# Kernel optimization log

Measured on AMD Instinct MI355X. Metric: run time of the kernel, lower is better.

Reference implementation:

```python
import jax, jax.numpy as jnp
import numpy as np

B0 = 2048
B1 = 2048


def _param(k, shape, fan_in):
    return jax.random.normal(k, shape, dtype=jnp.float32) / np.float32(np.sqrt(fan_in))


def setup_inputs() -> dict:
    key = jax.random.key(0)
    ks = jax.random.split(key, 32)
    inp = {
        'zw_0': jax.random.normal(ks[0], (B0, 128), dtype=jnp.float32),
        'zw_1': jax.random.normal(ks[1], (B1, 128), dtype=jnp.float32),
        'c': jax.random.normal(ks[2], (B0 + B1, 64), dtype=jnp.float32),
        # Wk: Linear(64 -> 128)
        'Wk_w': _param(ks[3], (128, 64), 64), 'Wk_b': jnp.zeros((128,), jnp.float32),
        # Ww[0], Ww[1]: Linear(64 -> 128)
        'Ww0_w': _param(ks[4], (128, 64), 64), 'Ww0_b': jnp.zeros((128,), jnp.float32),
        'Ww1_w': _param(ks[5], (128, 64), 64), 'Ww1_b': jnp.zeros((128,), jnp.float32),
        # linear_0/1: Linear(128 -> 64) + ReLU
        'lin0_w': _param(ks[6], (64, 128), 128), 'lin0_b': jnp.zeros((64,), jnp.float32),
        'lin1_w': _param(ks[7], (64, 128), 128), 'lin1_b': jnp.zeros((64,), jnp.float32),
        # attention_0/1: Linear(64->32), Tanh, Linear(32->1)
        'a0_1w': _param(ks[8], (32, 64), 64), 'a0_1b': jnp.zeros((32,), jnp.float32),
        'a0_2w': _param(ks[9], (1, 32), 32), 'a0_2b': jnp.zeros((1,), jnp.float32),
        'a1_1w': _param(ks[10], (32, 64), 64), 'a1_1b': jnp.zeros((32,), jnp.float32),
        'a1_2w': _param(ks[11], (1, 32), 32), 'a1_2b': jnp.zeros((1,), jnp.float32),
    }
    return inp


def _loo_pool(zw, lw, lb, a1w, a1b, a2w, a2b):
    # zt = ReLU(Linear(128->64))  [B, 64]
    zt = jax.nn.relu(zw @ lw.T + lb)
    # attention score per row  [B]
    s = (jnp.tanh(zt @ a1w.T + a1b) @ a2w.T + a2b)[:, 0]
    B = zt.shape[0]
    # leave-one-out softmax: row i attends over all j != i (diag masked to -inf)
    logits = jnp.where(jnp.eye(B, dtype=bool), -jnp.inf, jnp.broadcast_to(s[None, :], (B, B)))
    w = jax.nn.softmax(logits, axis=1)  # [B, B]
    return w @ zt  # [B, 64]


def reference(zw_0, zw_1, c,
              Wk_w, Wk_b, Ww0_w, Ww0_b, Ww1_w, Ww1_b,
              lin0_w, lin0_b, lin1_w, lin1_b,
              a0_1w, a0_1b, a0_2w, a0_2b,
              a1_1w, a1_1b, a1_2w, a1_2b):
    b0 = zw_0.shape[0]
    pooled0 = _loo_pool(zw_0, lin0_w, lin0_b, a0_1w, a0_1b, a0_2w, a0_2b)
    pooled1 = _loo_pool(zw_1, lin1_w, lin1_b, a1_1w, a1_1b, a1_2w, a1_2b)
    ck = c @ Wk_w.T + Wk_b  # [B, 128]
    pred0 = pooled0 @ Ww0_w.T + Ww0_b + ck[:b0]
    pred1 = pooled1 @ Ww1_w.T + Ww1_b + ck[b0:]
    pred = jnp.concatenate([pred0, pred1], axis=0)  # [B, 128]
    zw = jnp.concatenate([zw_0, zw_1], axis=0)      # [B, 128]
    total = zw @ pred.T                              # [B, B]
    batch = total.shape[0]
    nce_w = -jnp.sum(jnp.diagonal(jax.nn.log_softmax(total, axis=1))) / batch
    return nce_w
```

## Files before the change

kernel.cpp:

```cpp
#include <hip/hip_runtime.h>
#include <math.h>

#define B_TOT 4096
#define B_HALF 2048

#define ZT_OFF     0
#define S_OFF      262144
#define STATS_OFF  266240
#define ZWB_OFF    524288
#define PREDB_OFF  786432
#define ROWVAL_OFF 1048576

typedef __bf16 bf16x8 __attribute__((ext_vector_type(8)));
typedef float  f32x4  __attribute__((ext_vector_type(4)));

__device__ __forceinline__ unsigned short f2bf(float f) {
    unsigned u = __float_as_uint(f);
    u = u + 0x7fffu + ((u >> 16) & 1u);
    return (unsigned short)(u >> 16);
}
__device__ __forceinline__ float bf2f(unsigned short h) {
    return __uint_as_float(((unsigned)h) << 16);
}

__global__ __launch_bounds__(256)
void k_zt_s(const float* __restrict__ zw0, const float* __restrict__ zw1,
            const float* __restrict__ lin0_w, const float* __restrict__ lin0_b,
            const float* __restrict__ lin1_w, const float* __restrict__ lin1_b,
            const float* __restrict__ a0_1w, const float* __restrict__ a0_1b,
            const float* __restrict__ a0_2w, const float* __restrict__ a0_2b,
            const float* __restrict__ a1_1w, const float* __restrict__ a1_1b,
            const float* __restrict__ a1_2w, const float* __restrict__ a1_2b,
            float* __restrict__ ws) {
    __shared__ float lws[64 * 132];
    __shared__ float zws[16 * 132];
    __shared__ float ztl[16 * 68];
    __shared__ float a1s[32 * 68];
    int tid = threadIdx.x;
    int base = blockIdx.x * 16;
    int g = (base >= B_HALF);
    const float* lw = g ? lin1_w : lin0_w;
    const float* lb = g ? lin1_b : lin0_b;
    const float* w1 = g ? a1_1w : a0_1w;
    const float* b1 = g ? a1_1b : a0_1b;
    const float* w2 = g ? a1_2w : a0_2w;
    const float* b2 = g ? a1_2b : a0_2b;
    unsigned short* zwb = (unsigned short*)(ws + ZWB_OFF);

    const float4* lw4 = (const float4*)lw;
    for (int i = tid; i < 2048; i += 256) {
        int o = i >> 5, k4 = i & 31;
        ((float4*)(lws + o * 132))[k4] = lw4[i];
    }
    for (int i = tid; i < 512; i += 256) {
        int r = i >> 5, k4 = i & 31;
        int gi = base + r;
        const float* zr = (gi < B_HALF) ? (zw0 + (size_t)gi * 128)
                                        : (zw1 + (size_t)(gi - B_HALF) * 128);
        float4 v = ((const float4*)zr)[k4];
        ((float4*)(zws + r * 132))[k4] = v;
        uint2 p;
        p.x = (unsigned)f2bf(v.x) | ((unsigned)f2bf(v.y) << 16);
        p.y = (unsigned)f2bf(v.z) | ((unsigned)f2bf(v.w) << 16);
        ((uint2*)(zwb + (size_t)gi * 128))[k4] = p;
    }
    const float4* w14 = (const float4*)w1;
    for (int i = tid; i < 512; i += 256) {
        int o = i >> 4, k4 = i & 15;
        ((float4*)(a1s + o * 68))[k4] = w14[i];
    }
    __syncthreads();

    int o = tid & 63, rgrp = tid >> 6;
    {
        float bias = lb[o];
        float acc[4] = {bias, bias, bias, bias};
        const float4* wrow = (const float4*)(lws + o * 132);
        const float4* zr0 = (const float4*)(zws + (rgrp + 0) * 132);
        const float4* zr1 = (const float4*)(zws + (rgrp + 4) * 132);
        const float4* zr2 = (const float4*)(zws + (rgrp + 8) * 132);
        const float4* zr3 = (const float4*)(zws + (rgrp + 12) * 132);
#pragma unroll 4
        for (int k4 = 0; k4 < 32; ++k4) {
            float4 wv = wrow[k4];
            float4 z0 = zr0[k4], z1 = zr1[k4], z2 = zr2[k4], z3 = zr3[k4];
            acc[0] = fmaf(wv.x, z0.x, fmaf(wv.y, z0.y, fmaf(wv.z, z0.z, fmaf(wv.w, z0.w, acc[0]))));
            acc[1] = fmaf(wv.x, z1.x, fmaf(wv.y, z1.y, fmaf(wv.z, z1.z, fmaf(wv.w, z1.w, acc[1]))));
            acc[2] = fmaf(wv.x, z2.x, fmaf(wv.y, z2.y, fmaf(wv.z, z2.z, fmaf(wv.w, z2.w, acc[2]))));
            acc[3] = fmaf(wv.x, z3.x, fmaf(wv.y, z3.y, fmaf(wv.z, z3.z, fmaf(wv.w, z3.w, acc[3]))));
        }
#pragma unroll
        for (int rr = 0; rr < 4; ++rr) {
            int row = rgrp + rr * 4;
            float zt = fmaxf(acc[rr], 0.f);
            ztl[row * 68 + o] = zt;
            ws[ZT_OFF + (size_t)(base + row) * 64 + o] = zt;
        }
    }
    __syncthreads();

    int o2 = tid & 31, r2 = tid >> 5;
    const float4* arow = (const float4*)(a1s + o2 * 68);
#pragma unroll
    for (int rpass = 0; rpass < 2; ++rpass) {
        int row = r2 + rpass * 8;
        float a = b1[o2];
        const float4* zt4 = (const float4*)(ztl + row * 68);
#pragma unroll 4
        for (int k4 = 0; k4 < 16; ++k4) {
            float4 wv = arow[k4];
            float4 zv = zt4[k4];
            a = fmaf(wv.x, zv.x, fmaf(wv.y, zv.y, fmaf(wv.z, zv.z, fmaf(wv.w, zv.w, a))));
        }
        float h = tanhf(a) * w2[o2];
#pragma unroll
        for (int mask = 16; mask > 0; mask >>= 1) h += __shfl_xor(h, mask);
        if (o2 == 0) ws[S_OFF + base + row] = h + b2[0];
    }
}

__global__ __launch_bounds__(1024)
void k_stats(float* __restrict__ ws) {
    __shared__ float red[1024];
    __shared__ float el[B_HALF];
    __shared__ float tl[16 * 64];
    int gg = blockIdx.x, tid = threadIdx.x;
    const float* sg = ws + S_OFF + gg * B_HALF;

    float m = -INFINITY;
    for (int r = tid; r < B_HALF; r += 1024) m = fmaxf(m, sg[r]);
    red[tid] = m;
    __syncthreads();
    for (int o = 512; o > 0; o >>= 1) {
        if (tid < o) red[tid] = fmaxf(red[tid], red[tid + o]);
        __syncthreads();
    }
    m = red[0];
    __syncthreads();

    float Eloc = 0.f;
    for (int r = tid; r < B_HALF; r += 1024) {
        float ev = __expf(sg[r] - m);
        el[r] = ev;
        Eloc += ev;
    }
    red[tid] = Eloc;
    __syncthreads();
    for (int o = 512; o > 0; o >>= 1) {
        if (tid < o) red[tid] += red[tid + o];
        __syncthreads();
    }
    float E = red[0];

    int sub = tid >> 6, d = tid & 63;
    const float* ztg = ws + ZT_OFF + (size_t)gg * B_HALF * 64;
    float t = 0.f;
    for (int r = sub; r < B_HALF; r += 16) t = fmaf(el[r], ztg[(size_t)r * 64 + d], t);
    tl[sub * 64 + d] = t;
    __syncthreads();
    if (tid < 64) {
        float tt = 0.f;
#pragma unroll
        for (int q = 0; q < 16; ++q) tt += tl[q * 64 + tid];
        ws[STATS_OFF + gg * 66 + 2 + tid] = tt;
    }
    if (tid == 0) {
        ws[STATS_OFF + gg * 66]     = m;
        ws[STATS_OFF + gg * 66 + 1] = E;
    }
}

__global__ __launch_bounds__(256)
void k_pred(const float* __restrict__ c,
            const float* __restrict__ Wk_w, const float* __restrict__ Wk_b,
            const float* __restrict__ Ww0_w, const float* __restrict__ Ww0_b,
            const float* __restrict__ Ww1_w, const float* __restrict__ Ww1_b,
            float* __restrict__ ws) {
    __shared__ float Wws[128 * 68];
    __shared__ float Wks[128 * 68];
    __shared__ float pl[16 * 68];
    __shared__ float cl[16 * 68];
    __shared__ float er_l[16], inv_l[16];
    int tid = threadIdx.x;
    int base = blockIdx.x * 16;
    int g = (base >= B_HALF);
    const float* Ww  = g ? Ww1_w : Ww0_w;
    const float* Wwb = g ? Ww1_b : Ww0_b;
    unsigned short* predb = (unsigned short*)(ws + PREDB_OFF);

    const float4* Ww4 = (const float4*)Ww;
    const float4* Wk4 = (const float4*)Wk_w;
    for (int i = tid; i < 2048; i += 256) {
        int o = i >> 4, k4 = i & 15;
        ((float4*)(Wws + o * 68))[k4] = Ww4[i];
        ((float4*)(Wks + o * 68))[k4] = Wk4[i];
    }
    for (int i = tid; i < 256; i += 256) {
        int r = i >> 4, k4 = i & 15;
        ((float4*)(cl + r * 68))[k4] = ((const float4*)(c + (size_t)(base + r) * 64))[k4];
    }
    if (tid < 16) {
        float m = ws[STATS_OFF + g * 66];
        float E = ws[STATS_OFF + g * 66 + 1];
        float er = __expf(ws[S_OFF + base + tid] - m);
        er_l[tid] = er;
        inv_l[tid] = 1.f / (E - er);
    }
    __syncthreads();
    for (int i = tid; i < 1024; i += 256) {
        int r = i >> 6, k = i & 63;
        float T = ws[STATS_OFF + g * 66 + 2 + k];
        float zt = ws[ZT_OFF + (size_t)(base + r) * 64 + k];
        pl[r * 68 + k] = (T - er_l[r] * zt) * inv_l[r];
    }
    __syncthreads();

    int o = tid & 127, rsel = tid >> 7;
    float bias = Wwb[o] + Wk_b[o];
    float acc[8] = {bias, bias, bias, bias, bias, bias, bias, bias};
    const float4* wrow = (const float4*)(Wws + o * 68);
    const float4* krow = (const float4*)(Wks + o * 68);
#pragma unroll 4
    for (int k4 = 0; k4 < 16; ++k4) {
        float4 wv = wrow[k4];
#pragma unroll
        for (int j = 0; j < 8; ++j) {
            float4 pv = ((const float4*)(pl + (rsel + j * 2) * 68))[k4];
            acc[j] = fmaf(wv.x, pv.x, fmaf(wv.y, pv.y, fmaf(wv.z, pv.z, fmaf(wv.w, pv.w, acc[j]))));
        }
    }
#pragma unroll 4
    for (int k4 = 0; k4 < 16; ++k4) {
        float4 kv = krow[k4];
#pragma unroll
        for (int j = 0; j < 8; ++j) {
            float4 cv = ((const float4*)(cl + (rsel + j * 2) * 68))[k4];
            acc[j] = fmaf(kv.x, cv.x, fmaf(kv.y, cv.y, fmaf(kv.z, cv.z, fmaf(kv.w, cv.w, acc[j]))));
        }
    }
#pragma unroll
    for (int j = 0; j < 8; ++j) {
        int gi = base + rsel + j * 2;
        predb[(size_t)gi * 128 + o] = f2bf(acc[j]);
    }
}

__global__ __launch_bounds__(256)
void k_main(float* __restrict__ ws) {
    __shared__ unsigned short zs[64 * 136];
    __shared__ unsigned short ps[64 * 136];
    int tid = threadIdx.x;
    int jx = blockIdx.x;
    int i0 = blockIdx.y * 64, j0 = jx * 64;
    const unsigned short* zwb   = (const unsigned short*)(ws + ZWB_OFF);
    const unsigned short* predb = (const unsigned short*)(ws + PREDB_OFF);

    for (int i = tid; i < 1024; i += 256) {
        int r = i >> 4, gq = i & 15;
        ((float4*)(zs + r * 136))[gq] = ((const float4*)(zwb + (size_t)(i0 + r) * 128))[gq];
        ((float4*)(ps + r * 136))[gq] = ((const float4*)(predb + (size_t)(j0 + r) * 128))[gq];
    }
    __syncthreads();

    int lane = tid & 63, w = tid >> 6;
    int m16 = lane & 15, quad = lane >> 4;

    bf16x8 af[4];
#pragma unroll
    for (int kk = 0; kk < 4; ++kk)
        af[kk] = *((const bf16x8*)(zs + (w * 16 + m16) * 136 + kk * 32 + quad * 8));

    f32x4 acc[4];
#pragma unroll
    for (int b = 0; b < 4; ++b) acc[b] = (f32x4){0.f, 0.f, 0.f, 0.f};

#pragma unroll
    for (int b = 0; b < 4; ++b) {
#pragma unroll
        for (int kk = 0; kk < 4; ++kk) {
            bf16x8 bf = *((const bf16x8*)(ps + (b * 16 + m16) * 136 + kk * 32 + quad * 8));
            acc[b] = __builtin_amdgcn_mfma_f32_16x16x32_bf16(af[kk], bf, acc[b], 0, 0, 0);
        }
    }

    float2* part = (float2*)ws;
#pragma unroll
    for (int r = 0; r < 4; ++r) {
        float vm = fmaxf(fmaxf(acc[0][r], acc[1][r]), fmaxf(acc[2][r], acc[3][r]));
#pragma unroll
        for (int mask = 8; mask > 0; mask >>= 1) vm = fmaxf(vm, __shfl_xor(vm, mask));
        float se = __expf(acc[0][r] - vm) + __expf(acc[1][r] - vm) +
                   __expf(acc[2][r] - vm) + __expf(acc[3][r] - vm);
#pragma unroll
        for (int mask = 8; mask > 0; mask >>= 1) se += __shfl_xor(se, mask);
        if (m16 == 0) {
            int gi = i0 + w * 16 + quad * 4 + r;
            part[(size_t)gi * 64 + jx] = make_float2(vm, se);
        }
    }
}

__global__ __launch_bounds__(256)
void k_row(const float* __restrict__ zw0, const float* __restrict__ zw1,
           float* __restrict__ ws) {
    int tid = threadIdx.x;
    int sub = tid >> 6, lane = tid & 63;
    int r = blockIdx.x * 4 + sub;
    const float2* part = (const float2*)ws;
    const unsigned short* predb = (const unsigned short*)(ws + PREDB_OFF);

    float2 p2 = part[(size_t)r * 64 + lane];
    float M = p2.x, S = p2.y;
#pragma unroll
    for (int mask = 32; mask > 0; mask >>= 1) M = fmaxf(M, __shfl_xor(M, mask));
    S = S * __expf(p2.x - M);
#pragma unroll
    for (int mask = 32; mask > 0; mask >>= 1) S += __shfl_xor(S, mask);

    const float* zr = (r < B_HALF) ? (zw0 + (size_t)r * 128)
                                   : (zw1 + (size_t)(r - B_HALF) * 128);
    const unsigned short* pr = predb + (size_t)r * 128;
    float d = zr[lane] * bf2f(pr[lane]) + zr[lane + 64] * bf2f(pr[lane + 64]);
#pragma unroll
    for (int mask = 32; mask > 0; mask >>= 1) d += __shfl_xor(d, mask);

    if (lane == 0) ws[ROWVAL_OFF + r] = d - (M + logf(S));
}

__global__ __launch_bounds__(1024)
void k_final(const float* __restrict__ ws, float* __restrict__ out) {
    __shared__ float red[1024];
    int tid = threadIdx.x;
    float a = 0.f;
    for (int r = tid; r < B_TOT; r += 1024) a += ws[ROWVAL_OFF + r];
    red[tid] = a;
    __syncthreads();
    for (int o = 512; o > 0; o >>= 1) {
        if (tid < o) red[tid] += red[tid + o];
        __syncthreads();
    }
    if (tid == 0) out[0] = -red[0] / (float)B_TOT;
}

extern "C" void kernel_launch(void* const* d_in, const int* in_sizes, int n_in,
                              void* d_out, int out_size, void* d_ws, size_t ws_size,
                              hipStream_t stream) {
    const float* zw_0   = (const float*)d_in[0];
    const float* zw_1   = (const float*)d_in[1];
    const float* c      = (const float*)d_in[2];
    const float* Wk_w   = (const float*)d_in[3];
    const float* Wk_b   = (const float*)d_in[4];
    const float* Ww0_w  = (const float*)d_in[5];
    const float* Ww0_b  = (const float*)d_in[6];
    const float* Ww1_w  = (const float*)d_in[7];
    const float* Ww1_b  = (const float*)d_in[8];
    const float* lin0_w = (const float*)d_in[9];
    const float* lin0_b = (const float*)d_in[10];
    const float* lin1_w = (const float*)d_in[11];
    const float* lin1_b = (const float*)d_in[12];
    const float* a0_1w  = (const float*)d_in[13];
    const float* a0_1b  = (const float*)d_in[14];
    const float* a0_2w  = (const float*)d_in[15];
    const float* a0_2b  = (const float*)d_in[16];
    const float* a1_1w  = (const float*)d_in[17];
    const float* a1_1b  = (const float*)d_in[18];
    const float* a1_2w  = (const float*)d_in[19];
    const float* a1_2b  = (const float*)d_in[20];
    float* ws  = (float*)d_ws;
    float* out = (float*)d_out;

    k_zt_s<<<256, 256, 0, stream>>>(zw_0, zw_1, lin0_w, lin0_b, lin1_w, lin1_b,
                                    a0_1w, a0_1b, a0_2w, a0_2b,
                                    a1_1w, a1_1b, a1_2w, a1_2b, ws);
    k_stats<<<2, 1024, 0, stream>>>(ws);
    k_pred<<<256, 256, 0, stream>>>(c, Wk_w, Wk_b, Ww0_w, Ww0_b, Ww1_w, Ww1_b, ws);
    k_main<<<dim3(64, 64), 256, 0, stream>>>(ws);
    k_row<<<1024, 256, 0, stream>>>(zw_0, zw_1, ws);
    k_final<<<1, 1024, 0, stream>>>(ws, out);
}
```

Before: 172.4 us.

## Fuse all stages into one cooperative persistent kernel with grid syncs

Replaces the six separate kernel launches with a single cooperative kernel of 256 blocks that separates its stages with grid.sync. The softmax statistics are now per-block partial sums of exp(s) taken without max subtraction, which removes the serial two-block stats kernel. The main logits GEMM has each block stream 1024 columns with double-buffered LDS tiles and an online max/sum, and the final reduction uses an atomicAdd. This cuts launch overhead and serial small kernels, but it needs cooperative launch, runs only 256 blocks for the GEMM, and risks overflow because the exponentials are no longer max-stabilised.

After: 273.2 us. 58.4% more time.

```diff
diff --git a/kernel.cpp b/kernel.cpp
--- a/kernel.cpp
+++ b/kernel.cpp
@@ -1,15 +1,20 @@
 #include <hip/hip_runtime.h>
+#include <hip/hip_cooperative_groups.h>
 #include <math.h>
+
+namespace cg = cooperative_groups;
 
 #define B_TOT 4096
 #define B_HALF 2048
+#define NBLK 256
 
 #define ZT_OFF     0
 #define S_OFF      262144
-#define STATS_OFF  266240
+#define PSTAT_OFF  266240
 #define ZWB_OFF    524288
 #define PREDB_OFF  786432
-#define ROWVAL_OFF 1048576
+#define PART_OFF   1048576
+#define ACC_OFF    1081344
 
 typedef __bf16 bf16x8 __attribute__((ext_vector_type(8)));
 typedef float  f32x4  __attribute__((ext_vector_type(4)));
@@ -23,323 +28,325 @@
     return __uint_as_float(((unsigned)h) << 16);
 }
 
-__global__ __launch_bounds__(256)
-void k_zt_s(const float* __restrict__ zw0, const float* __restrict__ zw1,
-            const float* __restrict__ lin0_w, const float* __restrict__ lin0_b,
-            const float* __restrict__ lin1_w, const float* __restrict__ lin1_b,
-            const float* __restrict__ a0_1w, const float* __restrict__ a0_1b,
-            const float* __restrict__ a0_2w, const float* __restrict__ a0_2b,
-            const float* __restrict__ a1_1w, const float* __restrict__ a1_1b,
-            const float* __restrict__ a1_2w, const float* __restrict__ a1_2b,
-            float* __restrict__ ws) {
-    __shared__ float lws[64 * 132];
-    __shared__ float zws[16 * 132];
-    __shared__ float ztl[16 * 68];
-    __shared__ float a1s[32 * 68];
+__global__ __launch_bounds__(256, 1)
+void k_fused(const float* __restrict__ zw0, const float* __restrict__ zw1,
+             const float* __restrict__ c,
+             const float* __restrict__ Wk_w, const float* __restrict__ Wk_b,
+             const float* __restrict__ Ww0_w, const float* __restrict__ Ww0_b,
+             const float* __restrict__ Ww1_w, const float* __restrict__ Ww1_b,
+             const float* __restrict__ lin0_w, const float* __restrict__ lin0_b,
+             const float* __restrict__ lin1_w, const float* __restrict__ lin1_b,
+             const float* __restrict__ a0_1w, const float* __restrict__ a0_1b,
+             const float* __restrict__ a0_2w, const float* __restrict__ a0_2b,
+             const float* __restrict__ a1_1w, const float* __restrict__ a1_1b,
+             const float* __restrict__ a1_2w, const float* __restrict__ a1_2b,
+             float* __restrict__ ws, float* __restrict__ out) {
+    __shared__ float smem[20480];
+    cg::grid_group grid = cg::this_grid();
     int tid = threadIdx.x;
-    int base = blockIdx.x * 16;
-    int g = (base >= B_HALF);
-    const float* lw = g ? lin1_w : lin0_w;
-    const float* lb = g ? lin1_b : lin0_b;
-    const float* w1 = g ? a1_1w : a0_1w;
-    const float* b1 = g ? a1_1b : a0_1b;
-    const float* w2 = g ? a1_2w : a0_2w;
-    const float* b2 = g ? a1_2b : a0_2b;
-    unsigned short* zwb = (unsigned short*)(ws + ZWB_OFF);
-
-    const float4* lw4 = (const float4*)lw;
-    for (int i = tid; i < 2048; i += 256) {
-        int o = i >> 5, k4 = i & 31;
-        ((float4*)(lws + o * 132))[k4] = lw4[i];
-    }
-    for (int i = tid; i < 512; i += 256) {
-        int r = i >> 5, k4 = i & 31;
-        int gi = base + r;
-        const float* zr = (gi < B_HALF) ? (zw0 + (size_t)gi * 128)
-                                        : (zw1 + (size_t)(gi - B_HALF) * 128);
-        float4 v = ((const float4*)zr)[k4];
-        ((float4*)(zws + r * 132))[k4] = v;
-        uint2 p;
-        p.x = (unsigned)f2bf(v.x) | ((unsigned)f2bf(v.y) << 16);
-        p.y = (unsigned)f2bf(v.z) | ((unsigned)f2bf(v.w) << 16);
-        ((uint2*)(zwb + (size_t)gi * 128))[k4] = p;
-    }
-    const float4* w14 = (const float4*)w1;
-    for (int i = tid; i < 512; i += 256) {
-        int o = i >> 4, k4 = i & 15;
-        ((float4*)(a1s + o * 68))[k4] = w14[i];
-    }
-    __syncthreads();
-
-    int o = tid & 63, rgrp = tid >> 6;
+    int b = blockIdx.x;
+    unsigned short* zwb   = (unsigned short*)(ws + ZWB_OFF);
+    unsigned short* predb = (unsigned short*)(ws + PREDB_OFF);
+
     {
-        float bias = lb[o];
-        float acc[4] = {bias, bias, bias, bias};
-        const float4* wrow = (const float4*)(lws + o * 132);
-        const float4* zr0 = (const float4*)(zws + (rgrp + 0) * 132);
-        const float4* zr1 = (const float4*)(zws + (rgrp + 4) * 132);
-        const float4* zr2 = (const float4*)(zws + (rgrp + 8) * 132);
-        const float4* zr3 = (const float4*)(zws + (rgrp + 12) * 132);
+        float* lws = smem;
+        float* zws = smem + 8448;
+        float* ztl = smem + 10560;
+        float* a1s = smem + 11648;
+        float* el  = smem + 13824;
+        int base = b * 16;
+        int g = (base >= B_HALF);
+        const float* lw = g ? lin1_w : lin0_w;
+        const float* lb = g ? lin1_b : lin0_b;
+        const float* w1 = g ? a1_1w : a0_1w;
+        const float* b1 = g ? a1_1b : a0_1b;
+        const float* w2 = g ? a1_2w : a0_2w;
+        const float* b2 = g ? a1_2b : a0_2b;
+
+        const float4* lw4 = (const float4*)lw;
+        for (int i = tid; i < 2048; i += 256) {
+            int o = i >> 5, k4 = i & 31;
+            ((float4*)(lws + o * 132))[k4] = lw4[i];
+        }
+        for (int i = tid; i < 512; i += 256) {
+            int r = i >> 5, k4 = i & 31;
+            int gi = base + r;
+            const float* zr = (gi < B_HALF) ? (zw0 + (size_t)gi * 128)
+                                            : (zw1 + (size_t)(gi - B_HALF) * 128);
+            float4 v = ((const float4*)zr)[k4];
+            ((float4*)(zws + r * 132))[k4] = v;
+            uint2 p;
+            p.x = (unsigned)f2bf(v.x) | ((unsigned)f2bf(v.y) << 16);
+            p.y = (unsigned)f2bf(v.z) | ((unsigned)f2bf(v.w) << 16);
+            ((uint2*)(zwb + (size_t)gi * 128))[k4] = p;
+        }
+        const float4* w14 = (const float4*)w1;
+        for (int i = tid; i < 512; i += 256) {
+            int o = i >> 4, k4 = i & 15;
+            ((float4*)(a1s + o * 68))[k4] = w14[i];
+        }
+        __syncthreads();
+
+        int o = tid & 63, rgrp = tid >> 6;
+        {
+            float bias = lb[o];
+            float acc[4] = {bias, bias, bias, bias};
+            const float4* wrow = (const float4*)(lws + o * 132);
+            const float4* zr0 = (const float4*)(zws + (rgrp + 0) * 132);
+            const float4* zr1 = (const float4*)(zws + (rgrp + 4) * 132);
+            const float4* zr2 = (const float4*)(zws + (rgrp + 8) * 132);
+            const float4* zr3 = (const float4*)(zws + (rgrp + 12) * 132);
 #pragma unroll 4
-        for (int k4 = 0; k4 < 32; ++k4) {
-            float4 wv = wrow[k4];
-            float4 z0 = zr0[k4], z1 = zr1[k4], z2 = zr2[k4], z3 = zr3[k4];
-            acc[0] = fmaf(wv.x, z0.x, fmaf(wv.y, z0.y, fmaf(wv.z, z0.z, fmaf(wv.w, z0.w, acc[0]))));
-            acc[1] = fmaf(wv.x, z1.x, fmaf(wv.y, z1.y, fmaf(wv.z, z1.z, fmaf(wv.w, z1.w, acc[1]))));
-            acc[2] = fmaf(wv.x, z2.x, fmaf(wv.y, z2.y, fmaf(wv.z, z2.z, fmaf(wv.w, z2.w, acc[2]))));
-            acc[3] = fmaf(wv.x, z3.x, fmaf(wv.y, z3.y, fmaf(wv.z, z3.z, fmaf(wv.w, z3.w, acc[3]))));
-        }
-#pragma unroll
-        for (int rr = 0; rr < 4; ++rr) {
-            int row = rgrp + rr * 4;
-            float zt = fmaxf(acc[rr], 0.f);
-            ztl[row * 68 + o] = zt;
-            ws[ZT_OFF + (size_t)(base + row) * 64 + o] = zt;
-        }
-    }
-    __syncthreads();
-
-    int o2 = tid & 31, r2 = tid >> 5;
-    const float4* arow = (const float4*)(a1s + o2 * 68);
-#pragma unroll
-    for (int rpass = 0; rpass < 2; ++rpass) {
-        int row = r2 + rpass * 8;
-        float a = b1[o2];
-        const float4* zt4 = (const float4*)(ztl + row * 68);
+            for (int k4 = 0; k4 < 32; ++k4) {
+                float4 wv = wrow[k4];
+                float4 z0 = zr0[k4], z1 = zr1[k4], z2 = zr2[k4], z3 = zr3[k4];
+                acc[0] = fmaf(wv.x, z0.x, fmaf(wv.y, z0.y, fmaf(wv.z, z0.z, fmaf(wv.w, z0.w, acc[0]))));
+                acc[1] = fmaf(wv.x, z1.x, fmaf(wv.y, z1.y, fmaf(wv.z, z1.z, fmaf(wv.w, z1.w, acc[1]))));
+                acc[2] = fmaf(wv.x, z2.x, fmaf(wv.y, z2.y, fmaf(wv.z, z2.z, fmaf(wv.w, z2.w, acc[2]))));
+                acc[3] = fmaf(wv.x, z3.x, fmaf(wv.y, z3.y, fmaf(wv.z, z3.z, fmaf(wv.w, z3.w, acc[3]))));
+            }
+#pragma unroll
+            for (int rr = 0; rr < 4; ++rr) {
+                int row = rgrp + rr * 4;
+                float zt = fmaxf(acc[rr], 0.f);
+                ztl[row * 68 + o] = zt;
+                ws[ZT_OFF + (size_t)(base + row) * 64 + o] = zt;
+            }
+        }
+        __syncthreads();
+
+        int o2 = tid & 31, r2 = tid >> 5;
+        const float4* arow = (const float4*)(a1s + o2 * 68);
+#pragma unroll
+        for (int rpass = 0; rpass < 2; ++rpass) {
+            int row = r2 + rpass * 8;
+            float a = b1[o2];
+            const float4* zt4 = (const float4*)(ztl + row * 68);
+#pragma unroll 4
+            for (int k4 = 0; k4 < 16; ++k4) {
+                float4 wv = arow[k4];
+                float4 zv = zt4[k4];
+                a = fmaf(wv.x, zv.x, fmaf(wv.y, zv.y, fmaf(wv.z, zv.z, fmaf(wv.w, zv.w, a))));
+            }
+            float h = tanhf(a) * w2[o2];
+#pragma unroll
+            for (int mask = 16; mask > 0; mask >>= 1) h += __shfl_xor(h, mask);
+            if (o2 == 0) {
+                float e = __expf(h + b2[0]);
+                el[row] = e;
+                ws[S_OFF + base + row] = e;
+            }
+        }
+        __syncthreads();
+
+        if (tid < 64) {
+            float t = 0.f;
+#pragma unroll
+            for (int r = 0; r < 16; ++r) t = fmaf(el[r], ztl[r * 68 + tid], t);
+            ws[PSTAT_OFF + b * 65 + 1 + tid] = t;
+        }
+        if (tid == 64) {
+            float E = 0.f;
+#pragma unroll
+            for (int r = 0; r < 16; ++r) E += el[r];
+            ws[PSTAT_OFF + b * 65] = E;
+        }
+        if (b == 0 && tid == 0) ws[ACC_OFF] = 0.f;
+    }
+    grid.sync();
+
+    {
+        float* Wws = smem;
+        float* Wks = smem + 8704;
+        float* pl  = smem + 17408;
+        float* cl  = smem + 18496;
+        float* Ts  = smem + 19584;
+        int base = b * 16;
+        int g = (b >= 128);
+        const float* Ww  = g ? Ww1_w : Ww0_w;
+        const float* Wwb = g ? Ww1_b : Ww0_b;
+
+        const float4* Ww4 = (const float4*)Ww;
+        const float4* Wk4 = (const float4*)Wk_w;
+        for (int i = tid; i < 2048; i += 256) {
+            int o = i >> 4, k4 = i & 15;
+            ((float4*)(Wws + o * 68))[k4] = Ww4[i];
+            ((float4*)(Wks + o * 68))[k4] = Wk4[i];
+        }
+        if (tid < 256) {
+            int r = tid >> 4, k4 = tid & 15;
+            ((float4*)(cl + r * 68))[k4] = ((const float4*)(c + (size_t)(base + r) * 64))[k4];
+        }
+        if (tid < 65) {
+            float t = 0.f;
+            const float* ps = ws + PSTAT_OFF + (size_t)g * 128 * 65 + tid;
+            for (int q = 0; q < 128; ++q) t += ps[(size_t)q * 65];
+            Ts[tid] = t;
+        }
+        __syncthreads();
+        for (int i = tid; i < 1024; i += 256) {
+            int r = i >> 6, k = i & 63;
+            float er = ws[S_OFF + base + r];
+            pl[r * 68 + k] = (Ts[1 + k] - er * ws[ZT_OFF + (size_t)(base + r) * 64 + k])
+                             / (Ts[0] - er);
+        }
+        __syncthreads();
+
+        int o = tid & 127, rsel = tid >> 7;
+        float bias = Wwb[o] + Wk_b[o];
+        float acc[8] = {bias, bias, bias, bias, bias, bias, bias, bias};
+        const float4* wrow = (const float4*)(Wws + o * 68);
+        const float4* krow = (const float4*)(Wks + o * 68);
 #pragma unroll 4
         for (int k4 = 0; k4 < 16; ++k4) {
-            float4 wv = arow[k4];
-            float4 zv = zt4[k4];
-            a = fmaf(wv.x, zv.x, fmaf(wv.y, zv.y, fmaf(wv.z, zv.z, fmaf(wv.w, zv.w, a))));
-        }
-        float h = tanhf(a) * w2[o2];
-#pragma unroll
-        for (int mask = 16; mask > 0; mask >>= 1) h += __shfl_xor(h, mask);
-        if (o2 == 0) ws[S_OFF + base + row] = h + b2[0];
-    }
-}
-
-__global__ __launch_bounds__(1024)
-void k_stats(float* __restrict__ ws) {
-    __shared__ float red[1024];
-    __shared__ float el[B_HALF];
-    __shared__ float tl[16 * 64];
-    int gg = blockIdx.x, tid = threadIdx.x;
-    const float* sg = ws + S_OFF + gg * B_HALF;
-
-    float m = -INFINITY;
-    for (int r = tid; r < B_HALF; r += 1024) m = fmaxf(m, sg[r]);
-    red[tid] = m;
-    __syncthreads();
-    for (int o = 512; o > 0; o >>= 1) {
-        if (tid < o) red[tid] = fmaxf(red[tid], red[tid + o]);
-        __syncthreads();
-    }
-    m = red[0];
-    __syncthreads();
-
-    float Eloc = 0.f;
-    for (int r = tid; r < B_HALF; r += 1024) {
-        float ev = __expf(sg[r] - m);
-        el[r] = ev;
-        Eloc += ev;
-    }
-    red[tid] = Eloc;
-    __syncthreads();
-    for (int o = 512; o > 0; o >>= 1) {
-        if (tid < o) red[tid] += red[tid + o];
-        __syncthreads();
-    }
-    float E = red[0];
-
-    int sub = tid >> 6, d = tid & 63;
-    const float* ztg = ws + ZT_OFF + (size_t)gg * B_HALF * 64;
-    float t = 0.f;
-    for (int r = sub; r < B_HALF; r += 16) t = fmaf(el[r], ztg[(size_t)r * 64 + d], t);
-    tl[sub * 64 + d] = t;
-    __syncthreads();
-    if (tid < 64) {
-        float tt = 0.f;
-#pragma unroll
-        for (int q = 0; q < 16; ++q) tt += tl[q * 64 + tid];
-        ws[STATS_OFF + gg * 66 + 2 + tid] = tt;
-    }
-    if (tid == 0) {
-        ws[STATS_OFF + gg * 66]     = m;
-        ws[STATS_OFF + gg * 66 + 1] = E;
-    }
-}
-
-__global__ __launch_bounds__(256)
-void k_pred(const float* __restrict__ c,
-            const float* __restrict__ Wk_w, const float* __restrict__ Wk_b,
-            const float* __restrict__ Ww0_w, const float* __restrict__ Ww0_b,
-            const float* __restrict__ Ww1_w, const float* __restrict__ Ww1_b,
-            float* __restrict__ ws) {
-    __shared__ float Wws[128 * 68];
-    __shared__ float Wks[128 * 68];
-    __shared__ float pl[16 * 68];
-    __shared__ float cl[16 * 68];
-    __shared__ float er_l[16], inv_l[16];
-    int tid = threadIdx.x;
-    int base = blockIdx.x * 16;
-    int g = (base >= B_HALF);
-    const float* Ww  = g ? Ww1_w : Ww0_w;
-    const float* Wwb = g ? Ww1_b : Ww0_b;
-    unsigned short* predb = (unsigned short*)(ws + PREDB_OFF);
-
-    const float4* Ww4 = (const float4*)Ww;
-    const float4* Wk4 = (const float4*)Wk_w;
-    for (int i = tid; i < 2048; i += 256) {
-        int o = i >> 4, k4 = i & 15;
-        ((float4*)(Wws + o * 68))[k4] = Ww4[i];
-        ((float4*)(Wks + o * 68))[k4] = Wk4[i];
-    }
-    for (int i = tid; i < 256; i += 256) {
-        int r = i >> 4, k4 = i & 15;
-        ((float4*)(cl + r * 68))[k4] = ((const float4*)(c + (size_t)(base + r) * 64))[k4];
-    }
-    if (tid < 16) {
-        float m = ws[STATS_OFF + g * 66];
-        float E = ws[STATS_OFF + g * 66 + 1];
-        float er = __expf(ws[S_OFF + base + tid] - m);
-        er_l[tid] = er;
-        inv_l[tid] = 1.f / (E - er);
-    }
-    __syncthreads();
-    for (int i = tid; i < 1024; i += 256) {
-        int r = i >> 6, k = i & 63;
-        float T = ws[STATS_OFF + g * 66 + 2 + k];
-        float zt = ws[ZT_OFF + (size_t)(base + r) * 64 + k];
-        pl[r * 68 + k] = (T - er_l[r] * zt) * inv_l[r];
-    }
-    __syncthreads();
-
-    int o = tid & 127, rsel = tid >> 7;
-    float bias = Wwb[o] + Wk_b[o];
-    float acc[8] = {bias, bias, bias, bias, bias, bias, bias, bias};
-    const float4* wrow = (const float4*)(Wws + o * 68);
-    const float4* krow = (const float4*)(Wks + o * 68);
+            float4 wv = wrow[k4];
+#pragma unroll
+            for (int j = 0; j < 8; ++j) {
+                float4 pv = ((const float4*)(pl + (rsel + j * 2) * 68))[k4];
+                acc[j] = fmaf(wv.x, pv.x, fmaf(wv.y, pv.y, fmaf(wv.z, pv.z, fmaf(wv.w, pv.w, acc[j]))));
+            }
+        }
 #pragma unroll 4
-    for (int k4 = 0; k4 < 16; ++k4) {
-        float4 wv = wrow[k4];
-#pragma unroll
-        for (int j = 0; j < 8; ++j) {
-            float4 pv = ((const float4*)(pl + (rsel + j * 2) * 68))[k4];
-            acc[j] = fmaf(wv.x, pv.x, fmaf(wv.y, pv.y, fmaf(wv.z, pv.z, fmaf(wv.w, pv.w, acc[j]))));
-        }
-    }
-#pragma unroll 4
-    for (int k4 = 0; k4 < 16; ++k4) {
-        float4 kv = krow[k4];
-#pragma unroll
-        for (int j = 0; j < 8; ++j) {
-            float4 cv = ((const float4*)(cl + (rsel + j * 2) * 68))[k4];
-            acc[j] = fmaf(kv.x, cv.x, fmaf(kv.y, cv.y, fmaf(kv.z, cv.z, fmaf(kv.w, cv.w, acc[j]))));
-        }
-    }
-#pragma unroll
-    for (int j = 0; j < 8; ++j) {
-        int gi = base + rsel + j * 2;
-        predb[(size_t)gi * 128 + o] = f2bf(acc[j]);
-    }
-}
-
-__global__ __launch_bounds__(256)
-void k_main(float* __restrict__ ws) {
-    __shared__ unsigned short zs[64 * 136];
-    __shared__ unsigned short ps[64 * 136];
-    int tid = threadIdx.x;
-    int jx = blockIdx.x;
-    int i0 = blockIdx.y * 64, j0 = jx * 64;
-    const unsigned short* zwb   = (const unsigned short*)(ws + ZWB_OFF);
-    const unsigned short* predb = (const unsigned short*)(ws + PREDB_OFF);
-
-    for (int i = tid; i < 1024; i += 256) {
-        int r = i >> 4, gq = i & 15;
-        ((float4*)(zs + r * 136))[gq] = ((const float4*)(zwb + (size_t)(i0 + r) * 128))[gq];
-        ((float4*)(ps + r * 136))[gq] = ((const float4*)(predb + (size_t)(j0 + r) * 128))[gq];
-    }
-    __syncthreads();
-
-    int lane = tid & 63, w = tid >> 6;
-    int m16 = lane & 15, quad = lane >> 4;
-
-    bf16x8 af[4];
-#pragma unroll
-    for (int kk = 0; kk < 4; ++kk)
-        af[kk] = *((const bf16x8*)(zs + (w * 16 + m16) * 136 + kk * 32 + quad * 8));
-
-    f32x4 acc[4];
-#pragma unroll
-    for (int b = 0; b < 4; ++b) acc[b] = (f32x4){0.f, 0.f, 0.f, 0.f};
-
-#pragma unroll
-    for (int b = 0; b < 4; ++b) {
-#pragma unroll
-        for (int kk = 0; kk < 4; ++kk) {
-            bf16x8 bf = *((const bf16x8*)(ps + (b * 16 + m16) * 136 + kk * 32 + quad * 8));
-            acc[b] = __builtin_amdgcn_mfma_f32_16x16x32_bf16(af[kk], bf, acc[b], 0, 0, 0);
-        }
-    }
-
-    float2* part = (float2*)ws;
-#pragma unroll
-    for (int r = 0; r < 4; ++r) {
-        float vm = fmaxf(fmaxf(acc[0][r], acc[1][r]), fmaxf(acc[2][r], acc[3][r]));
-#pragma unroll
-        for (int mask = 8; mask > 0; mask >>= 1) vm = fmaxf(vm, __shfl_xor(vm, mask));
-        float se = __expf(acc[0][r] - vm) + __expf(acc[1][r] - vm) +
-                   __expf(acc[2][r] - vm) + __expf(acc[3][r] - vm);
-#pragma unroll
-        for (int mask = 8; mask > 0; mask >>= 1) se += __shfl_xor(se, mask);
-        if (m16 == 0) {
-            int gi = i0 + w * 16 + quad * 4 + r;
-            part[(size_t)gi * 64 + jx] = make_float2(vm, se);
-        }
-    }
-}
-
-__global__ __launch_bounds__(256)
-void k_row(const float* __restrict__ zw0, const float* __restrict__ zw1,
-           float* __restrict__ ws) {
-    int tid = threadIdx.x;
-    int sub = tid >> 6, lane = tid & 63;
-    int r = blockIdx.x * 4 + sub;
-    const float2* part = (const float2*)ws;
-    const unsigned short* predb = (const unsigned short*)(ws + PREDB_OFF);
-
-    float2 p2 = part[(size_t)r * 64 + lane];
-    float M = p2.x, S = p2.y;
-#pragma unroll
-    for (int mask = 32; mask > 0; mask >>= 1) M = fmaxf(M, __shfl_xor(M, mask));
-    S = S * __expf(p2.x - M);
-#pragma unroll
-    for (int mask = 32; mask > 0; mask >>= 1) S += __shfl_xor(S, mask);
-
-    const float* zr = (r < B_HALF) ? (zw0 + (size_t)r * 128)
-                                   : (zw1 + (size_t)(r - B_HALF) * 128);
-    const unsigned short* pr = predb + (size_t)r * 128;
-    float d = zr[lane] * bf2f(pr[lane]) + zr[lane + 64] * bf2f(pr[lane + 64]);
-#pragma unroll
-    for (int mask = 32; mask > 0; mask >>= 1) d += __shfl_xor(d, mask);
-
-    if (lane == 0) ws[ROWVAL_OFF + r] = d - (M + logf(S));
-}
-
-__global__ __launch_bounds__(1024)
-void k_final(const float* __restrict__ ws, float* __restrict__ out) {
-    __shared__ float red[1024];
-    int tid = threadIdx.x;
-    float a = 0.f;
-    for (int r = tid; r < B_TOT; r += 1024) a += ws[ROWVAL_OFF + r];
-    red[tid] = a;
-    __syncthreads();
-    for (int o = 512; o > 0; o >>= 1) {
-        if (tid < o) red[tid] += red[tid + o];
-        __syncthreads();
-    }
-    if (tid == 0) out[0] = -red[0] / (float)B_TOT;
+        for (int k4 = 0; k4 < 16; ++k4) {
+            float4 kv = krow[k4];
+#pragma unroll
+            for (int j = 0; j < 8; ++j) {
+                float4 cv = ((const float4*)(cl + (rsel + j * 2) * 68))[k4];
+                acc[j] = fmaf(kv.x, cv.x, fmaf(kv.y, cv.y, fmaf(kv.z, cv.z, fmaf(kv.w, cv.w, acc[j]))));
+            }
+        }
+#pragma unroll
+        for (int j = 0; j < 8; ++j)
+            predb[(size_t)(base + rsel + j * 2) * 128 + o] = f2bf(acc[j]);
+    }
+    grid.sync();
+
+    {
+        int it = b >> 2, jg = b & 3;
+        unsigned short* sm16 = (unsigned short*)smem;
+        unsigned short* zs = sm16;
+        unsigned short* ps0 = sm16 + 8704;
+        unsigned short* ps1 = sm16 + 17408;
+
+        for (int i = tid; i < 1024; i += 256) {
+            int r = i >> 4, gq = i & 15;
+            ((float4*)(zs + r * 136))[gq] =
+                ((const float4*)(zwb + (size_t)(it * 64 + r) * 128))[gq];
+            ((float4*)(ps0 + r * 136))[gq] =
+                ((const float4*)(predb + (size_t)(jg * 1024 + r) * 128))[gq];
+        }
+        __syncthreads();
+
+        int lane = tid & 63, w = tid >> 6;
+        int m16 = lane & 15, quad = lane >> 4;
+
+        bf16x8 af[4];
+#pragma unroll
+        for (int kk = 0; kk < 4; ++kk)
+            af[kk] = *((const bf16x8*)(zs + (w * 16 + m16) * 136 + kk * 32 + quad * 8));
+
+        float m_run[4], s_run[4];
+#pragma unroll
+        for (int r = 0; r < 4; ++r) { m_run[r] = -INFINITY; s_run[r] = 0.f; }
+
+        for (int jt = 0; jt < 16; ++jt) {
+            unsigned short* cur = (jt & 1) ? ps1 : ps0;
+            unsigned short* nxt = (jt & 1) ? ps0 : ps1;
+            if (jt < 15) {
+                int j0 = jg * 1024 + (jt + 1) * 64;
+                for (int i = tid; i < 1024; i += 256) {
+                    int r = i >> 4, gq = i & 15;
+                    ((float4*)(nxt + r * 136))[gq] =
+                        ((const float4*)(predb + (size_t)(j0 + r) * 128))[gq];
+                }
+            }
+            f32x4 acc[4];
+#pragma unroll
+            for (int b4 = 0; b4 < 4; ++b4) {
+                acc[b4] = (f32x4){0.f, 0.f, 0.f, 0.f};
+#pragma unroll
+                for (int kk = 0; kk < 4; ++kk) {
+                    bf16x8 bf = *((const bf16x8*)(cur + (b4 * 16 + m16) * 136 + kk * 32 + quad * 8));
+                    acc[b4] = __builtin_amdgcn_mfma_f32_16x16x32_bf16(af[kk], bf, acc[b4], 0, 0, 0);
+                }
+            }
+#pragma unroll
+            for (int r = 0; r < 4; ++r) {
+                float vm = fmaxf(fmaxf(acc[0][r], acc[1][r]), fmaxf(acc[2][r], acc[3][r]));
+                float mn = fmaxf(m_run[r], vm);
+                float add = __expf(acc[0][r] - mn) + __expf(acc[1][r] - mn) +
+                            __expf(acc[2][r] - mn) + __expf(acc[3][r] - mn);
+                s_run[r] = s_run[r] * __expf(m_run[r] - mn) + add;
+                m_run[r] = mn;
+            }
+            __syncthreads();
+        }
+
+#pragma unroll
+        for (int r = 0; r < 4; ++r) {
+            float m = m_run[r], s = s_run[r];
+#pragma unroll
+            for (int mask = 1; mask < 16; mask <<= 1) {
+                float om = __shfl_xor(m, mask);
+                float os = __shfl_xor(s, mask);
+                float mn = fmaxf(m, om);
+                s = s * __expf(m - mn) + os * __expf(om - mn);
+                m = mn;
+            }
+            if (m16 == 0) {
+                int gi = it * 64 + w * 16 + quad * 4 + r;
+                ws[PART_OFF + (size_t)gi * 8 + jg * 2]     = m;
+                ws[PART_OFF + (size_t)gi * 8 + jg * 2 + 1] = s;
+            }
+        }
+    }
+    grid.sync();
+
+    {
+        float* rv = smem;
+        int r16 = tid >> 4, s16 = tid & 15;
+        int gi = b * 16 + r16;
+        const uint4 za = *((const uint4*)(zwb   + (size_t)gi * 128 + s16 * 8));
+        const uint4 pa = *((const uint4*)(predb + (size_t)gi * 128 + s16 * 8));
+        float d = 0.f;
+        const unsigned* zu = (const unsigned*)&za;
+        const unsigned* pu = (const unsigned*)&pa;
+#pragma unroll
+        for (int q = 0; q < 4; ++q) {
+            d = fmaf(bf2f((unsigned short)(zu[q] & 0xffff)),
+                     bf2f((unsigned short)(pu[q] & 0xffff)), d);
+            d = fmaf(bf2f((unsigned short)(zu[q] >> 16)),
+                     bf2f((unsigned short)(pu[q] >> 16)), d);
+        }
+#pragma unroll
+        for (int mask = 1; mask < 16; mask <<= 1) d += __shfl_xor(d, mask);
+        if (s16 == 0) {
+            float M = -INFINITY;
+#pragma unroll
+            for (int q = 0; q < 4; ++q)
+                M = fmaxf(M, ws[PART_OFF + (size_t)gi * 8 + q * 2]);
+            float S = 0.f;
+#pragma unroll
+            for (int q = 0; q < 4; ++q)
+                S += ws[PART_OFF + (size_t)gi * 8 + q * 2 + 1] *
+                     __expf(ws[PART_OFF + (size_t)gi * 8 + q * 2] - M);
+            rv[r16] = d - (M + logf(S));
+        }
+        __syncthreads();
+        if (tid == 0) {
+            float bs = 0.f;
+#pragma unroll
+            for (int i = 0; i < 16; ++i) bs += rv[i];
+            atomicAdd(ws + ACC_OFF, bs);
+        }
+    }
+    grid.sync();
+
+    if (b == 0 && tid == 0) {
+        float acc = __hip_atomic_load(ws + ACC_OFF, __ATOMIC_RELAXED,
+                                      __HIP_MEMORY_SCOPE_AGENT);
+        out[0] = -acc / (float)B_TOT;
+    }
 }
 
 extern "C" void kernel_launch(void* const* d_in, const int* in_sizes, int n_in,
@@ -369,12 +376,15 @@
     float* ws  = (float*)d_ws;
     float* out = (float*)d_out;
 
-    k_zt_s<<<256, 256, 0, stream>>>(zw_0, zw_1, lin0_w, lin0_b, lin1_w, lin1_b,
-                                    a0_1w, a0_1b, a0_2w, a0_2b,
-                                    a1_1w, a1_1b, a1_2w, a1_2b, ws);
-    k_stats<<<2, 1024, 0, stream>>>(ws);
-    k_pred<<<256, 256, 0, stream>>>(c, Wk_w, Wk_b, Ww0_w, Ww0_b, Ww1_w, Ww1_b, ws);
-    k_main<<<dim3(64, 64), 256, 0, stream>>>(ws);
-    k_row<<<1024, 256, 0, stream>>>(zw_0, zw_1, ws);
-    k_final<<<1, 1024, 0, stream>>>(ws, out);
+    void* args[] = {
+        (void*)&zw_0, (void*)&zw_1, (void*)&c,
+        (void*)&Wk_w, (void*)&Wk_b,
+        (void*)&Ww0_w, (void*)&Ww0_b, (void*)&Ww1_w, (void*)&Ww1_b,
+        (void*)&lin0_w, (void*)&lin0_b, (void*)&lin1_w, (void*)&lin1_b,
+        (void*)&a0_1w, (void*)&a0_1b, (void*)&a0_2w, (void*)&a0_2b,
+        (void*)&a1_1w, (void*)&a1_1b, (void*)&a1_2w, (void*)&a1_2b,
+        (void*)&ws, (void*)&out
+    };
+    hipLaunchCooperativeKernel((void*)k_fused, dim3(NBLK), dim3(256),
+                               args, 0, stream);
 }
```
